# Kernel optimization log

Measured on AMD Instinct MI355X. Metric: run time of the kernel, lower is better.

## Reference

```python
import jax, jax.numpy as jnp
import numpy as np

D_MODEL = 512
N_HEADS = 8
D_HEAD = D_MODEL // N_HEADS
SCALE = 1.0 / np.sqrt(D_MODEL).astype(np.float32)  # source divides by sqrt(d_model), not sqrt(d_head)


def setup_inputs() -> dict:
    key = jax.random.key(0)
    ks = jax.random.split(key, 9)
    B, S = 4, 2048
    std = 1.0 / np.sqrt(D_MODEL).astype(np.float32)
    x = jax.random.normal(ks[0], (B, S, D_MODEL), dtype=jnp.float32)
    Wq = jax.random.normal(ks[1], (D_MODEL, D_MODEL), dtype=jnp.float32) * std
    bq = jnp.zeros((D_MODEL,), jnp.float32)
    Wk = jax.random.normal(ks[2], (D_MODEL, D_MODEL), dtype=jnp.float32) * std
    bk = jnp.zeros((D_MODEL,), jnp.float32)
    Wv = jax.random.normal(ks[3], (D_MODEL, D_MODEL), dtype=jnp.float32) * std
    bv = jnp.zeros((D_MODEL,), jnp.float32)
    Wo = jax.random.normal(ks[4], (D_MODEL, D_MODEL), dtype=jnp.float32) * std
    bo = jnp.zeros((D_MODEL,), jnp.float32)
    return {"x": x, "Wq": Wq, "bq": bq, "Wk": Wk, "bk": bk,
            "Wv": Wv, "bv": bv, "Wo": Wo, "bo": bo}


def reference(x, Wq, bq, Wk, bk, Wv, bv, Wo, bo):
    B, S, _ = x.shape
    # projections -> [B, H, S, Dh]
    def split_heads(t):
        return t.reshape(B, S, N_HEADS, D_HEAD).transpose(0, 2, 1, 3)
    q = split_heads(x @ Wq + bq)
    k = split_heads(x @ Wk + bk)
    v = split_heads(x @ Wv + bv)
    # scores: [B, H, S, S], scaled by 1/sqrt(d_model) as in source
    scores = jnp.einsum('bhqd,bhkd->bhqk', q, k) * SCALE
    weights = jax.nn.softmax(scores, axis=-1)
    # dropout is identity at inference time
    att = jnp.einsum('bhqk,bhkd->bhqd', weights, v)
    att = att.transpose(0, 2, 1, 3).reshape(B, S, D_MODEL)
    return att @ Wo + bo
```

## Files before the change

kernel.cpp:

```cpp
#include <hip/hip_runtime.h>
#include <math.h>

#define BATCH   4
#define S_LEN   2048
#define DMODEL  512
#define NHEADS  8
#define DHEAD   64
#define M_TOT   8192
#define ATT_SCALE 0.04419417382415922f
#define QSCALE (ATT_SCALE * 1.44269504088896f)

using short8  = __attribute__((ext_vector_type(8))) short;
using floatx4 = __attribute__((ext_vector_type(4))) float;

__device__ __forceinline__ ushort f2bf(float f) {
    union { float f; unsigned u; } x; x.f = f;
    unsigned u = x.u + 0x7FFFu + ((x.u >> 16) & 1u);
    return (ushort)(u >> 16);
}
__device__ __forceinline__ unsigned pk2(float a, float b) {
    return (unsigned)f2bf(a) | ((unsigned)f2bf(b) << 16);
}
__device__ __forceinline__ unsigned pkr2(float a, float b) {
    unsigned ua = __float_as_uint(a) + 0x8000u;
    unsigned ub = __float_as_uint(b) + 0x8000u;
    return __builtin_amdgcn_perm(ub, ua, 0x07060302u);
}

__global__ __launch_bounds__(256) void prep(
    const float* __restrict__ x,
    const float* __restrict__ Wq, const float* __restrict__ Wk,
    const float* __restrict__ Wv, const float* __restrict__ Wo,
    ushort* __restrict__ xb, ushort* __restrict__ WT)
{
    const int bid = blockIdx.x;
    if (bid < 4096) {
        const int i = (bid * 256 + threadIdx.x) * 4;
        float4 f = *(const float4*)(x + i);
        uint2 o; o.x = pk2(f.x, f.y); o.y = pk2(f.z, f.w);
        *(uint2*)(xb + i) = o;
    } else {
        const int rb = bid - 4096;
        const int p  = rb >> 6;
        const int rem = rb & 63;
        const int n  = (rem >> 5) * 256 + threadIdx.x;
        const int k0 = (rem & 31) * 16;
        const float* W = (p == 0) ? Wq : (p == 1) ? Wk : (p == 2) ? Wv : Wo;
        unsigned u[8];
        #pragma unroll
        for (int j = 0; j < 8; ++j) {
            float a = W[(k0 + 2 * j)     * DMODEL + n];
            float b = W[(k0 + 2 * j + 1) * DMODEL + n];
            u[j] = pk2(a, b);
        }
        ushort* dst = WT + ((size_t)p * DMODEL + n) * DMODEL + k0;
        *(uint4*)dst       = *(uint4*)&u[0];
        *(uint4*)(dst + 8) = *(uint4*)&u[4];
    }
}

__global__ __launch_bounds__(256, 4) void qkv_gemm(
    const ushort* __restrict__ xb, const ushort* __restrict__ WT,
    const float* __restrict__ bq, const float* __restrict__ bk, const float* __restrict__ bv,
    ushort* __restrict__ q, ushort* __restrict__ k, ushort* __restrict__ vT)
{
    __shared__ ushort SMEM[128 * 136];
    ushort (*A)[40] = (ushort(*)[40])SMEM;
    ushort (*B)[40] = (ushort(*)[40])(SMEM + 128 * 40);
    ushort (*CT)[136] = (ushort(*)[136])SMEM;

    const int tid = threadIdx.x;
    const int wv  = tid >> 6, lane = tid & 63, l16 = lane & 15, quad = lane >> 4;
    const int m0  = blockIdx.x * 128;
    const int ng0 = blockIdx.y * 128;
    const int p   = ng0 >> 9;
    const int n0  = ng0 & 511;
    const ushort* Wp  = WT + (size_t)p * DMODEL * DMODEL + (size_t)n0 * DMODEL;
    const float* bias = (p == 0) ? bq : (p == 1) ? bk : bv;
    const float scl   = (p == 0) ? QSCALE : 1.0f;

    const int wm = (wv & 1) * 64, wn = (wv >> 1) * 64;
    floatx4 acc[4][4] = {};
    const int ar = tid >> 1, ac = (tid & 1) * 16;

    for (int k0 = 0; k0 < DMODEL; k0 += 32) {
        uint4 a0 = *(const uint4*)(xb + (size_t)(m0 + ar) * DMODEL + k0 + ac);
        uint4 a1 = *(const uint4*)(xb + (size_t)(m0 + ar) * DMODEL + k0 + ac + 8);
        uint4 b0 = *(const uint4*)(Wp + (size_t)ar * DMODEL + k0 + ac);
        uint4 b1 = *(const uint4*)(Wp + (size_t)ar * DMODEL + k0 + ac + 8);
        *(uint4*)&A[ar][ac] = a0; *(uint4*)&A[ar][ac + 8] = a1;
        *(uint4*)&B[ar][ac] = b0; *(uint4*)&B[ar][ac + 8] = b1;
        __syncthreads();

        short8 af[4], bf[4];
        #pragma unroll
        for (int i = 0; i < 4; ++i) af[i] = *(const short8*)&A[wm + i * 16 + l16][quad * 8];
        #pragma unroll
        for (int c = 0; c < 4; ++c) bf[c] = *(const short8*)&B[wn + c * 16 + l16][quad * 8];
        #pragma unroll
        for (int i = 0; i < 4; ++i)
            #pragma unroll
            for (int c = 0; c < 4; ++c)
                acc[i][c] = __builtin_amdgcn_mfma_f32_16x16x32_bf16(af[i], bf[c], acc[i][c], 0, 0, 0);
        __syncthreads();
    }

    if (p < 2) {
        #pragma unroll
        for (int c = 0; c < 4; ++c) {
            const int n = n0 + wn + c * 16 + l16;
            const float bb = bias[n];
            const int h = n >> 6, dh = n & 63;
            #pragma unroll
            for (int i = 0; i < 4; ++i)
                #pragma unroll
                for (int r = 0; r < 4; ++r) {
                    const int m = m0 + wm + i * 16 + quad * 4 + r;
                    const int b = m >> 11, s = m & 2047;
                    const ushort val = f2bf((acc[i][c][r] + bb) * scl);
                    if (p == 0) q[((size_t)(b * NHEADS + h) * S_LEN + s) * DHEAD + dh] = val;
                    else        k[((size_t)(b * NHEADS + h) * S_LEN + s) * DHEAD + dh] = val;
                }
        }
    } else {
        #pragma unroll
        for (int c = 0; c < 4; ++c) {
            const int n = wn + c * 16 + l16;
            const float bb = bias[n0 + n];
            #pragma unroll
            for (int i = 0; i < 4; ++i) {
                uint2 o;
                o.x = pk2(acc[i][c][0] + bb, acc[i][c][1] + bb);
                o.y = pk2(acc[i][c][2] + bb, acc[i][c][3] + bb);
                *(uint2*)&CT[n][wm + i * 16 + quad * 4] = o;
            }
        }
        __syncthreads();
        const int n  = tid >> 1, mh = (tid & 1) * 64;
        const int gn = n0 + n;
        const int h  = gn >> 6, dh = gn & 63;
        const int b  = m0 >> 11, sb = (m0 & 2047) + mh;
        ushort* dst = vT + ((size_t)(b * NHEADS + h) * DHEAD + dh) * S_LEN + sb;
        #pragma unroll
        for (int j = 0; j < 8; ++j)
            *(uint4*)(dst + j * 8) = *(const uint4*)&CT[n][mh + j * 8];
    }
}

__global__ __launch_bounds__(256, 4) void attn(
    const ushort* __restrict__ Q, const ushort* __restrict__ K,
    const ushort* __restrict__ vT, ushort* __restrict__ att,
    float* __restrict__ Opart, float* __restrict__ Lpart,
    const int KT, const int direct)
{
    __shared__ ushort Klds[64][72];
    __shared__ ushort Vt[64][72];
    __shared__ ushort Plds[128][72];

    const int tid = threadIdx.x;
    const int wv  = tid >> 6, lane = tid & 63, l16 = lane & 15, quad = lane >> 4;
    const int q0  = blockIdx.x * 128;
    const int bh  = blockIdx.y;
    const int ck  = blockIdx.z;
    const int kbase = ck * KT;
    const ushort* Qh = Q  + (size_t)bh * S_LEN * DHEAD;
    const ushort* Kh = K  + (size_t)bh * S_LEN * DHEAD;
    const ushort* Vh = vT + (size_t)bh * DHEAD * S_LEN;

    short8 qf[2][2];
    #pragma unroll
    for (int ni = 0; ni < 2; ++ni) {
        const ushort* qrow = Qh + (size_t)(q0 + wv * 32 + ni * 16 + l16) * DHEAD;
        qf[0][ni] = *(const short8*)(qrow + quad * 8);
        qf[1][ni] = *(const short8*)(qrow + 32 + quad * 8);
    }

    floatx4 oacc[4][2] = {};
    float lsum[2] = {0.f, 0.f};

    const int srow = tid >> 2, sc0 = (tid & 3) * 16;
    uint4 ka, kb, va, vb;
    {
        const ushort* Ks = Kh + (size_t)(kbase * 64 + srow) * DHEAD + sc0;
        const ushort* Vs = Vh + (size_t)srow * S_LEN + kbase * 64 + sc0;
        ka = *(const uint4*)Ks; kb = *(const uint4*)(Ks + 8);
        va = *(const uint4*)Vs; vb = *(const uint4*)(Vs + 8);
    }

    for (int kt = 0; kt < KT; ++kt) {
        *(uint4*)&Klds[srow][sc0] = ka; *(uint4*)&Klds[srow][sc0 + 8] = kb;
        *(uint4*)&Vt[srow][sc0]   = va; *(uint4*)&Vt[srow][sc0 + 8]   = vb;
        __syncthreads();

        if (kt + 1 < KT) {
            const ushort* Ks = Kh + (size_t)((kbase + kt + 1) * 64 + srow) * DHEAD + sc0;
            const ushort* Vs = Vh + (size_t)srow * S_LEN + (kbase + kt + 1) * 64 + sc0;
            ka = *(const uint4*)Ks; kb = *(const uint4*)(Ks + 8);
            va = *(const uint4*)Vs; vb = *(const uint4*)(Vs + 8);
        }

        floatx4 sc[4][2] = {};
        #pragma unroll
        for (int s = 0; s < 2; ++s)
            #pragma unroll
            for (int mi = 0; mi < 4; ++mi) {
                short8 kf = *(const short8*)&Klds[mi * 16 + l16][s * 32 + quad * 8];
                #pragma unroll
                for (int ni = 0; ni < 2; ++ni)
                    sc[mi][ni] = __builtin_amdgcn_mfma_f32_16x16x32_bf16(kf, qf[s][ni], sc[mi][ni], 0, 0, 0);
            }

        #pragma unroll
        for (int mi = 0; mi < 4; ++mi)
            #pragma unroll
            for (int ni = 0; ni < 2; ++ni) {
                const float p0 = __builtin_amdgcn_exp2f(sc[mi][ni][0]);
                const float p1 = __builtin_amdgcn_exp2f(sc[mi][ni][1]);
                const float p2 = __builtin_amdgcn_exp2f(sc[mi][ni][2]);
                const float p3 = __builtin_amdgcn_exp2f(sc[mi][ni][3]);
                lsum[ni] += (p0 + p1) + (p2 + p3);
                uint2 o; o.x = pkr2(p0, p1); o.y = pkr2(p2, p3);
                *(uint2*)&Plds[wv * 32 + ni * 16 + l16][mi * 16 + quad * 4] = o;
            }

        #pragma unroll
        for (int s = 0; s < 2; ++s) {
            short8 pf[2];
            #pragma unroll
            for (int ni = 0; ni < 2; ++ni)
                pf[ni] = *(const short8*)&Plds[wv * 32 + ni * 16 + l16][s * 32 + quad * 8];
            #pragma unroll
            for (int mi = 0; mi < 4; ++mi) {
                short8 vf = *(const short8*)&Vt[mi * 16 + l16][s * 32 + quad * 8];
                #pragma unroll
                for (int ni = 0; ni < 2; ++ni)
                    oacc[mi][ni] = __builtin_amdgcn_mfma_f32_16x16x32_bf16(vf, pf[ni], oacc[mi][ni], 0, 0, 0);
            }
        }
        __syncthreads();
    }

    float tot[2];
    #pragma unroll
    for (int ni = 0; ni < 2; ++ni) {
        float t = lsum[ni];
        t += __shfl_xor(t, 16, 64);
        t += __shfl_xor(t, 32, 64);
        tot[ni] = t;
    }

    if (direct) {
        const int b = bh >> 3, h = bh & 7;
        #pragma unroll
        for (int ni = 0; ni < 2; ++ni) {
            const float inv = 1.f / tot[ni];
            const int qi = q0 + wv * 32 + ni * 16 + l16;
            ushort* dst = att + ((size_t)(b * S_LEN + qi)) * DMODEL + h * DHEAD;
            #pragma unroll
            for (int mi = 0; mi < 4; ++mi) {
                uint2 o;
                o.x = pk2(oacc[mi][ni][0] * inv, oacc[mi][ni][1] * inv);
                o.y = pk2(oacc[mi][ni][2] * inv, oacc[mi][ni][3] * inv);
                *(uint2*)(dst + mi * 16 + quad * 4) = o;
            }
        }
    } else {
        #pragma unroll
        for (int ni = 0; ni < 2; ++ni) {
            const int qi = q0 + wv * 32 + ni * 16 + l16;
            const size_t row = (size_t)(ck * 32 + bh) * S_LEN + qi;
            if (quad == 0) Lpart[row] = tot[ni];
            #pragma unroll
            for (int mi = 0; mi < 4; ++mi) {
                float4 o = { oacc[mi][ni][0], oacc[mi][ni][1],
                             oacc[mi][ni][2], oacc[mi][ni][3] };
                *(float4*)&Opart[row * DHEAD + mi * 16 + quad * 4] = o;
            }
        }
    }
}

__global__ __launch_bounds__(256) void combine(
    const float* __restrict__ Opart, const float* __restrict__ Lpart,
    ushort* __restrict__ att)
{
    const int idx = blockIdx.x * 256 + threadIdx.x;
    const int row = idx >> 3;
    const int dho = (idx & 7) * 8;
    const int bh = row >> 11, qq = row & 2047;
    const float* o0 = Opart + (size_t)row * DHEAD + dho;
    const float* o1 = Opart + (size_t)(65536 + row) * DHEAD + dho;
    float4 a0 = *(const float4*)o0,       a1 = *(const float4*)(o0 + 4);
    float4 b0 = *(const float4*)o1,       b1 = *(const float4*)(o1 + 4);
    const float inv = 1.f / (Lpart[row] + Lpart[65536 + row]);
    uint4 u;
    u.x = pk2((a0.x + b0.x) * inv, (a0.y + b0.y) * inv);
    u.y = pk2((a0.z + b0.z) * inv, (a0.w + b0.w) * inv);
    u.z = pk2((a1.x + b1.x) * inv, (a1.y + b1.y) * inv);
    u.w = pk2((a1.z + b1.z) * inv, (a1.w + b1.w) * inv);
    ushort* dst = att + ((size_t)((bh >> 3) * S_LEN + qq)) * DMODEL + (bh & 7) * DHEAD + dho;
    *(uint4*)dst = u;
}

__global__ __launch_bounds__(256, 4) void out_gemm(
    const ushort* __restrict__ att, const ushort* __restrict__ WoT,
    const float* __restrict__ bo, float* __restrict__ out)
{
    __shared__ ushort A[128][40];
    __shared__ ushort B[128][40];

    const int tid = threadIdx.x;
    const int wv  = tid >> 6, lane = tid & 63, l16 = lane & 15, quad = lane >> 4;
    const int m0 = blockIdx.x * 128;
    const int n0 = blockIdx.y * 128;

    const int wm = (wv & 1) * 64, wn = (wv >> 1) * 64;
    floatx4 acc[4][4] = {};
    const int ar = tid >> 1, ac = (tid & 1) * 16;

    for (int k0 = 0; k0 < DMODEL; k0 += 32) {
        uint4 a0 = *(const uint4*)(att + (size_t)(m0 + ar) * DMODEL + k0 + ac);
        uint4 a1 = *(const uint4*)(att + (size_t)(m0 + ar) * DMODEL + k0 + ac + 8);
        uint4 b0 = *(const uint4*)(WoT + (size_t)(n0 + ar) * DMODEL + k0 + ac);
        uint4 b1 = *(const uint4*)(WoT + (size_t)(n0 + ar) * DMODEL + k0 + ac + 8);
        *(uint4*)&A[ar][ac] = a0; *(uint4*)&A[ar][ac + 8] = a1;
        *(uint4*)&B[ar][ac] = b0; *(uint4*)&B[ar][ac + 8] = b1;
        __syncthreads();

        short8 af[4], bf[4];
        #pragma unroll
        for (int i = 0; i < 4; ++i) af[i] = *(const short8*)&A[wm + i * 16 + l16][quad * 8];
        #pragma unroll
        for (int c = 0; c < 4; ++c) bf[c] = *(const short8*)&B[wn + c * 16 + l16][quad * 8];
        #pragma unroll
        for (int i = 0; i < 4; ++i)
            #pragma unroll
            for (int c = 0; c < 4; ++c)
                acc[i][c] = __builtin_amdgcn_mfma_f32_16x16x32_bf16(af[i], bf[c], acc[i][c], 0, 0, 0);
        __syncthreads();
    }

    #pragma unroll
    for (int c = 0; c < 4; ++c) {
        const int n = n0 + wn + c * 16 + l16;
        const float bb = bo[n];
        #pragma unroll
        for (int i = 0; i < 4; ++i)
            #pragma unroll
            for (int r = 0; r < 4; ++r) {
                const int m = m0 + wm + i * 16 + quad * 4 + r;
                out[(size_t)m * DMODEL + n] = acc[i][c][r] + bb;
            }
    }
}

extern "C" void kernel_launch(void* const* d_in, const int* in_sizes, int n_in,
                              void* d_out, int out_size, void* d_ws, size_t ws_size,
                              hipStream_t stream)
{
    const float* x  = (const float*)d_in[0];
    const float* Wq = (const float*)d_in[1];
    const float* bq = (const float*)d_in[2];
    const float* Wk = (const float*)d_in[3];
    const float* bk = (const float*)d_in[4];
    const float* Wv = (const float*)d_in[5];
    const float* bv = (const float*)d_in[6];
    const float* Wo = (const float*)d_in[7];
    const float* bo = (const float*)d_in[8];
    float* out = (float*)d_out;

    ushort* ws = (ushort*)d_ws;
    const size_t SZ = (size_t)M_TOT * DMODEL;
    ushort* xb  = ws;
    ushort* att = ws;
    ushort* WT  = ws + SZ;
    ushort* q   = WT + 4 * (size_t)DMODEL * DMODEL;
    ushort* k   = q + SZ;
    ushort* vT  = k + SZ;
    float*  Opart = (float*)(vT + SZ);
    float*  Lpart = Opart + 2 * (size_t)32 * S_LEN * DHEAD;

    const size_t base_need  = (size_t)(vT + SZ - ws) * 2;
    const size_t split_need = base_need + 2 * ((size_t)32 * S_LEN * DHEAD + 32 * S_LEN) * 4;
    const int SPLIT = (ws_size >= split_need) ? 2 : 1;

    prep<<<4096 + 256, 256, 0, stream>>>(x, Wq, Wk, Wv, Wo, xb, WT);

    qkv_gemm<<<dim3(M_TOT / 128, 3 * DMODEL / 128), 256, 0, stream>>>(
        xb, WT, bq, bk, bv, q, k, vT);

    attn<<<dim3(S_LEN / 128, BATCH * NHEADS, SPLIT), 256, 0, stream>>>(
        q, k, vT, att, Opart, Lpart, S_LEN / 64 / SPLIT, SPLIT == 1 ? 1 : 0);

    if (SPLIT == 2)
        combine<<<(32 * S_LEN * DHEAD / 8) / 256, 256, 0, stream>>>(Opart, Lpart, att);

    out_gemm<<<dim3(M_TOT / 128, DMODEL / 128), 256, 0, stream>>>(
        att, WT + 3 * (size_t)DMODEL * DMODEL, bo, out);
}
```

Before: 181.8 us.

## Fuse split-K combine into out GEMM, keep P in registers, double-buffer attention K/V

```diff
diff --git a/kernel.cpp b/kernel.cpp
--- a/kernel.cpp
+++ b/kernel.cpp
@@ -11,6 +11,7 @@
 #define QSCALE (ATT_SCALE * 1.44269504088896f)
 
 using short8  = __attribute__((ext_vector_type(8))) short;
+using short4v = __attribute__((ext_vector_type(4))) short;
 using floatx4 = __attribute__((ext_vector_type(4))) float;
 
 __device__ __forceinline__ ushort f2bf(float f) {
@@ -83,14 +84,23 @@
     floatx4 acc[4][4] = {};
     const int ar = tid >> 1, ac = (tid & 1) * 16;
 
+    uint4 pa0, pa1, pb0, pb1;
+    pa0 = *(const uint4*)(xb + (size_t)(m0 + ar) * DMODEL + ac);
+    pa1 = *(const uint4*)(xb + (size_t)(m0 + ar) * DMODEL + ac + 8);
+    pb0 = *(const uint4*)(Wp + (size_t)ar * DMODEL + ac);
+    pb1 = *(const uint4*)(Wp + (size_t)ar * DMODEL + ac + 8);
+
     for (int k0 = 0; k0 < DMODEL; k0 += 32) {
-        uint4 a0 = *(const uint4*)(xb + (size_t)(m0 + ar) * DMODEL + k0 + ac);
-        uint4 a1 = *(const uint4*)(xb + (size_t)(m0 + ar) * DMODEL + k0 + ac + 8);
-        uint4 b0 = *(const uint4*)(Wp + (size_t)ar * DMODEL + k0 + ac);
-        uint4 b1 = *(const uint4*)(Wp + (size_t)ar * DMODEL + k0 + ac + 8);
-        *(uint4*)&A[ar][ac] = a0; *(uint4*)&A[ar][ac + 8] = a1;
-        *(uint4*)&B[ar][ac] = b0; *(uint4*)&B[ar][ac + 8] = b1;
-        __syncthreads();
+        *(uint4*)&A[ar][ac] = pa0; *(uint4*)&A[ar][ac + 8] = pa1;
+        *(uint4*)&B[ar][ac] = pb0; *(uint4*)&B[ar][ac + 8] = pb1;
+        __syncthreads();
+
+        if (k0 + 32 < DMODEL) {
+            pa0 = *(const uint4*)(xb + (size_t)(m0 + ar) * DMODEL + k0 + 32 + ac);
+            pa1 = *(const uint4*)(xb + (size_t)(m0 + ar) * DMODEL + k0 + 32 + ac + 8);
+            pb0 = *(const uint4*)(Wp + (size_t)ar * DMODEL + k0 + 32 + ac);
+            pb1 = *(const uint4*)(Wp + (size_t)ar * DMODEL + k0 + 32 + ac + 8);
+        }
 
         short8 af[4], bf[4];
         #pragma unroll
@@ -149,13 +159,11 @@
 
 __global__ __launch_bounds__(256, 4) void attn(
     const ushort* __restrict__ Q, const ushort* __restrict__ K,
-    const ushort* __restrict__ vT, ushort* __restrict__ att,
-    float* __restrict__ Opart, float* __restrict__ Lpart,
-    const int KT, const int direct)
-{
-    __shared__ ushort Klds[64][72];
-    __shared__ ushort Vt[64][72];
-    __shared__ ushort Plds[128][72];
+    const ushort* __restrict__ vT,
+    float* __restrict__ Opart, float* __restrict__ Lpart, const int KT)
+{
+    __shared__ ushort Klds[2][64][72];
+    __shared__ ushort Vt[2][64][72];
 
     const int tid = threadIdx.x;
     const int wv  = tid >> 6, lane = tid & 63, l16 = lane & 15, quad = lane >> 4;
@@ -188,8 +196,9 @@
     }
 
     for (int kt = 0; kt < KT; ++kt) {
-        *(uint4*)&Klds[srow][sc0] = ka; *(uint4*)&Klds[srow][sc0 + 8] = kb;
-        *(uint4*)&Vt[srow][sc0]   = va; *(uint4*)&Vt[srow][sc0 + 8]   = vb;
+        const int buf = kt & 1;
+        *(uint4*)&Klds[buf][srow][sc0] = ka; *(uint4*)&Klds[buf][srow][sc0 + 8] = kb;
+        *(uint4*)&Vt[buf][srow][sc0]   = va; *(uint4*)&Vt[buf][srow][sc0 + 8]   = vb;
         __syncthreads();
 
         if (kt + 1 < KT) {
@@ -199,45 +208,45 @@
             va = *(const uint4*)Vs; vb = *(const uint4*)(Vs + 8);
         }
 
-        floatx4 sc[4][2] = {};
-        #pragma unroll
-        for (int s = 0; s < 2; ++s)
-            #pragma unroll
-            for (int mi = 0; mi < 4; ++mi) {
-                short8 kf = *(const short8*)&Klds[mi * 16 + l16][s * 32 + quad * 8];
+        #pragma unroll
+        for (int mi = 0; mi < 4; ++mi) {
+            floatx4 s0 = {}, s1 = {};
+            #pragma unroll
+            for (int s = 0; s < 2; ++s) {
+                short8 kf = *(const short8*)&Klds[buf][mi * 16 + l16][s * 32 + quad * 8];
+                s0 = __builtin_amdgcn_mfma_f32_16x16x32_bf16(kf, qf[s][0], s0, 0, 0, 0);
+                s1 = __builtin_amdgcn_mfma_f32_16x16x32_bf16(kf, qf[s][1], s1, 0, 0, 0);
+            }
+            short4v vfr[4];
+            #pragma unroll
+            for (int c = 0; c < 4; ++c)
+                vfr[c] = *(const short4v*)&Vt[buf][c * 16 + l16][mi * 16 + quad * 4];
+
+            {
+                const float p0 = __builtin_amdgcn_exp2f(s0[0]);
+                const float p1 = __builtin_amdgcn_exp2f(s0[1]);
+                const float p2 = __builtin_amdgcn_exp2f(s0[2]);
+                const float p3 = __builtin_amdgcn_exp2f(s0[3]);
+                lsum[0] += (p0 + p1) + (p2 + p3);
+                uint2 o; o.x = pkr2(p0, p1); o.y = pkr2(p2, p3);
+                short4v pf; *(uint2*)&pf = o;
                 #pragma unroll
-                for (int ni = 0; ni < 2; ++ni)
-                    sc[mi][ni] = __builtin_amdgcn_mfma_f32_16x16x32_bf16(kf, qf[s][ni], sc[mi][ni], 0, 0, 0);
+                for (int c = 0; c < 4; ++c)
+                    oacc[c][0] = __builtin_amdgcn_mfma_f32_16x16x16bf16_1k(vfr[c], pf, oacc[c][0], 0, 0, 0);
             }
-
-        #pragma unroll
-        for (int mi = 0; mi < 4; ++mi)
-            #pragma unroll
-            for (int ni = 0; ni < 2; ++ni) {
-                const float p0 = __builtin_amdgcn_exp2f(sc[mi][ni][0]);
-                const float p1 = __builtin_amdgcn_exp2f(sc[mi][ni][1]);
-                const float p2 = __builtin_amdgcn_exp2f(sc[mi][ni][2]);
-                const float p3 = __builtin_amdgcn_exp2f(sc[mi][ni][3]);
-                lsum[ni] += (p0 + p1) + (p2 + p3);
+            {
+                const float p0 = __builtin_amdgcn_exp2f(s1[0]);
+                const float p1 = __builtin_amdgcn_exp2f(s1[1]);
+                const float p2 = __builtin_amdgcn_exp2f(s1[2]);
+                const float p3 = __builtin_amdgcn_exp2f(s1[3]);
+                lsum[1] += (p0 + p1) + (p2 + p3);
                 uint2 o; o.x = pkr2(p0, p1); o.y = pkr2(p2, p3);
-                *(uint2*)&Plds[wv * 32 + ni * 16 + l16][mi * 16 + quad * 4] = o;
+                short4v pf; *(uint2*)&pf = o;
+                #pragma unroll
+                for (int c = 0; c < 4; ++c)
+                    oacc[c][1] = __builtin_amdgcn_mfma_f32_16x16x16bf16_1k(vfr[c], pf, oacc[c][1], 0, 0, 0);
             }
-
-        #pragma unroll
-        for (int s = 0; s < 2; ++s) {
-            short8 pf[2];
-            #pragma unroll
-            for (int ni = 0; ni < 2; ++ni)
-                pf[ni] = *(const short8*)&Plds[wv * 32 + ni * 16 + l16][s * 32 + quad * 8];
-            #pragma unroll
-            for (int mi = 0; mi < 4; ++mi) {
-                short8 vf = *(const short8*)&Vt[mi * 16 + l16][s * 32 + quad * 8];
-                #pragma unroll
-                for (int ni = 0; ni < 2; ++ni)
-                    oacc[mi][ni] = __builtin_amdgcn_mfma_f32_16x16x32_bf16(vf, pf[ni], oacc[mi][ni], 0, 0, 0);
-            }
-        }
-        __syncthreads();
+        }
     }
 
     float tot[2];
@@ -249,108 +258,83 @@
         tot[ni] = t;
     }
 
-    if (direct) {
-        const int b = bh >> 3, h = bh & 7;
-        #pragma unroll
-        for (int ni = 0; ni < 2; ++ni) {
-            const float inv = 1.f / tot[ni];
-            const int qi = q0 + wv * 32 + ni * 16 + l16;
-            ushort* dst = att + ((size_t)(b * S_LEN + qi)) * DMODEL + h * DHEAD;
-            #pragma unroll
-            for (int mi = 0; mi < 4; ++mi) {
-                uint2 o;
-                o.x = pk2(oacc[mi][ni][0] * inv, oacc[mi][ni][1] * inv);
-                o.y = pk2(oacc[mi][ni][2] * inv, oacc[mi][ni][3] * inv);
-                *(uint2*)(dst + mi * 16 + quad * 4) = o;
-            }
-        }
-    } else {
-        #pragma unroll
-        for (int ni = 0; ni < 2; ++ni) {
-            const int qi = q0 + wv * 32 + ni * 16 + l16;
-            const size_t row = (size_t)(ck * 32 + bh) * S_LEN + qi;
-            if (quad == 0) Lpart[row] = tot[ni];
-            #pragma unroll
-            for (int mi = 0; mi < 4; ++mi) {
-                float4 o = { oacc[mi][ni][0], oacc[mi][ni][1],
-                             oacc[mi][ni][2], oacc[mi][ni][3] };
-                *(float4*)&Opart[row * DHEAD + mi * 16 + quad * 4] = o;
-            }
-        }
-    }
-}
-
-__global__ __launch_bounds__(256) void combine(
+    #pragma unroll
+    for (int ni = 0; ni < 2; ++ni) {
+        const int qi = q0 + wv * 32 + ni * 16 + l16;
+        const size_t row = (size_t)(ck * 32 + bh) * S_LEN + qi;
+        if (quad == 0) Lpart[row] = tot[ni];
+        #pragma unroll
+        for (int mi = 0; mi < 4; ++mi) {
+            float4 o = { oacc[mi][ni][0], oacc[mi][ni][1],
+                         oacc[mi][ni][2], oacc[mi][ni][3] };
+            *(float4*)&Opart[row * DHEAD + mi * 16 + quad * 4] = o;
+        }
+    }
+}
+
+__global__ __launch_bounds__(256, 4) void out_gemm(
     const float* __restrict__ Opart, const float* __restrict__ Lpart,
-    ushort* __restrict__ att)
-{
-    const int idx = blockIdx.x * 256 + threadIdx.x;
-    const int row = idx >> 3;
-    const int dho = (idx & 7) * 8;
-    const int bh = row >> 11, qq = row & 2047;
-    const float* o0 = Opart + (size_t)row * DHEAD + dho;
-    const float* o1 = Opart + (size_t)(65536 + row) * DHEAD + dho;
-    float4 a0 = *(const float4*)o0,       a1 = *(const float4*)(o0 + 4);
-    float4 b0 = *(const float4*)o1,       b1 = *(const float4*)(o1 + 4);
-    const float inv = 1.f / (Lpart[row] + Lpart[65536 + row]);
-    uint4 u;
-    u.x = pk2((a0.x + b0.x) * inv, (a0.y + b0.y) * inv);
-    u.y = pk2((a0.z + b0.z) * inv, (a0.w + b0.w) * inv);
-    u.z = pk2((a1.x + b1.x) * inv, (a1.y + b1.y) * inv);
-    u.w = pk2((a1.z + b1.z) * inv, (a1.w + b1.w) * inv);
-    ushort* dst = att + ((size_t)((bh >> 3) * S_LEN + qq)) * DMODEL + (bh & 7) * DHEAD + dho;
-    *(uint4*)dst = u;
-}
-
-__global__ __launch_bounds__(256, 4) void out_gemm(
-    const ushort* __restrict__ att, const ushort* __restrict__ WoT,
-    const float* __restrict__ bo, float* __restrict__ out)
-{
-    __shared__ ushort A[128][40];
+    const ushort* __restrict__ WoT, const float* __restrict__ bo,
+    float* __restrict__ out)
+{
+    __shared__ ushort A[64][40];
     __shared__ ushort B[128][40];
 
     const int tid = threadIdx.x;
     const int wv  = tid >> 6, lane = tid & 63, l16 = lane & 15, quad = lane >> 4;
-    const int m0 = blockIdx.x * 128;
+    const int m0 = blockIdx.x * 64;
     const int n0 = blockIdx.y * 128;
 
-    const int wm = (wv & 1) * 64, wn = (wv >> 1) * 64;
-    floatx4 acc[4][4] = {};
-    const int ar = tid >> 1, ac = (tid & 1) * 16;
+    const int ar = tid >> 2, ac = (tid & 3) * 8;
+    const int am = m0 + ar, ab = am >> 11, aq = am & 2047;
+    float invl[NHEADS];
+    #pragma unroll
+    for (int h = 0; h < NHEADS; ++h) {
+        const size_t rw = (size_t)(ab * NHEADS + h) * S_LEN + aq;
+        invl[h] = 1.f / (Lpart[rw] + Lpart[65536 + rw]);
+    }
+    const int br = tid >> 1, bc = (tid & 1) * 16;
+
+    floatx4 acc[8] = {};
 
     for (int k0 = 0; k0 < DMODEL; k0 += 32) {
-        uint4 a0 = *(const uint4*)(att + (size_t)(m0 + ar) * DMODEL + k0 + ac);
-        uint4 a1 = *(const uint4*)(att + (size_t)(m0 + ar) * DMODEL + k0 + ac + 8);
-        uint4 b0 = *(const uint4*)(WoT + (size_t)(n0 + ar) * DMODEL + k0 + ac);
-        uint4 b1 = *(const uint4*)(WoT + (size_t)(n0 + ar) * DMODEL + k0 + ac + 8);
-        *(uint4*)&A[ar][ac] = a0; *(uint4*)&A[ar][ac + 8] = a1;
-        *(uint4*)&B[ar][ac] = b0; *(uint4*)&B[ar][ac + 8] = b1;
-        __syncthreads();
-
-        short8 af[4], bf[4];
-        #pragma unroll
-        for (int i = 0; i < 4; ++i) af[i] = *(const short8*)&A[wm + i * 16 + l16][quad * 8];
-        #pragma unroll
-        for (int c = 0; c < 4; ++c) bf[c] = *(const short8*)&B[wn + c * 16 + l16][quad * 8];
-        #pragma unroll
-        for (int i = 0; i < 4; ++i)
-            #pragma unroll
-            for (int c = 0; c < 4; ++c)
-                acc[i][c] = __builtin_amdgcn_mfma_f32_16x16x32_bf16(af[i], bf[c], acc[i][c], 0, 0, 0);
-        __syncthreads();
-    }
-
-    #pragma unroll
-    for (int c = 0; c < 4; ++c) {
-        const int n = n0 + wn + c * 16 + l16;
+        const int kk = k0 + ac, h = kk >> 6, dh = kk & 63;
+        const float* p0 = Opart + ((size_t)(ab * NHEADS + h) * S_LEN + aq) * DHEAD + dh;
+        const float* p1 = p0 + (size_t)65536 * DHEAD;
+        float4 a0 = *(const float4*)p0,       a1 = *(const float4*)(p0 + 4);
+        float4 c0 = *(const float4*)p1,       c1 = *(const float4*)(p1 + 4);
+        const float iv = invl[h];
+        uint2 u0, u1;
+        u0.x = pk2((a0.x + c0.x) * iv, (a0.y + c0.y) * iv);
+        u0.y = pk2((a0.z + c0.z) * iv, (a0.w + c0.w) * iv);
+        u1.x = pk2((a1.x + c1.x) * iv, (a1.y + c1.y) * iv);
+        u1.y = pk2((a1.z + c1.z) * iv, (a1.w + c1.w) * iv);
+        *(uint2*)&A[ar][ac]     = u0;
+        *(uint2*)&A[ar][ac + 4] = u1;
+
+        uint4 b0 = *(const uint4*)(WoT + (size_t)(n0 + br) * DMODEL + k0 + bc);
+        uint4 b1 = *(const uint4*)(WoT + (size_t)(n0 + br) * DMODEL + k0 + bc + 8);
+        *(uint4*)&B[br][bc] = b0; *(uint4*)&B[br][bc + 8] = b1;
+        __syncthreads();
+
+        short8 af = *(const short8*)&A[wv * 16 + l16][quad * 8];
+        #pragma unroll
+        for (int c = 0; c < 8; ++c) {
+            short8 bf = *(const short8*)&B[c * 16 + l16][quad * 8];
+            acc[c] = __builtin_amdgcn_mfma_f32_16x16x32_bf16(af, bf, acc[c], 0, 0, 0);
+        }
+        __syncthreads();
+    }
+
+    #pragma unroll
+    for (int c = 0; c < 8; ++c) {
+        const int n = n0 + c * 16 + l16;
         const float bb = bo[n];
         #pragma unroll
-        for (int i = 0; i < 4; ++i)
-            #pragma unroll
-            for (int r = 0; r < 4; ++r) {
-                const int m = m0 + wm + i * 16 + quad * 4 + r;
-                out[(size_t)m * DMODEL + n] = acc[i][c][r] + bb;
-            }
+        for (int r = 0; r < 4; ++r) {
+            const int m = m0 + wv * 16 + quad * 4 + r;
+            out[(size_t)m * DMODEL + n] = acc[c][r] + bb;
+        }
     }
 }
 
@@ -372,7 +356,6 @@
     ushort* ws = (ushort*)d_ws;
     const size_t SZ = (size_t)M_TOT * DMODEL;
     ushort* xb  = ws;
-    ushort* att = ws;
     ushort* WT  = ws + SZ;
     ushort* q   = WT + 4 * (size_t)DMODEL * DMODEL;
     ushort* k   = q + SZ;
@@ -380,21 +363,14 @@
     float*  Opart = (float*)(vT + SZ);
     float*  Lpart = Opart + 2 * (size_t)32 * S_LEN * DHEAD;
 
-    const size_t base_need  = (size_t)(vT + SZ - ws) * 2;
-    const size_t split_need = base_need + 2 * ((size_t)32 * S_LEN * DHEAD + 32 * S_LEN) * 4;
-    const int SPLIT = (ws_size >= split_need) ? 2 : 1;
-
     prep<<<4096 + 256, 256, 0, stream>>>(x, Wq, Wk, Wv, Wo, xb, WT);
 
     qkv_gemm<<<dim3(M_TOT / 128, 3 * DMODEL / 128), 256, 0, stream>>>(
         xb, WT, bq, bk, bv, q, k, vT);
 
-    attn<<<dim3(S_LEN / 128, BATCH * NHEADS, SPLIT), 256, 0, stream>>>(
-        q, k, vT, att, Opart, Lpart, S_LEN / 64 / SPLIT, SPLIT == 1 ? 1 : 0);
-
-    if (SPLIT == 2)
-        combine<<<(32 * S_LEN * DHEAD / 8) / 256, 256, 0, stream>>>(Opart, Lpart, att);
-
-    out_gemm<<<dim3(M_TOT / 128, DMODEL / 128), 256, 0, stream>>>(
-        att, WT + 3 * (size_t)DMODEL * DMODEL, bo, out);
-}
+    attn<<<dim3(S_LEN / 128, BATCH * NHEADS, 2), 256, 0, stream>>>(
+        q, k, vT, Opart, Lpart, S_LEN / 64 / 2);
+
+    out_gemm<<<dim3(M_TOT / 64, DMODEL / 128), 256, 0, stream>>>(
+        Opart, Lpart, WT + 3 * (size_t)DMODEL * DMODEL, bo, out);
+}
```

New measurement: 177.5 us. 2.4% less time.
